# Kernel optimization log

Hardware: AMD Instinct MI355X
Metric: run time of the kernel (lower is better)

The kernel has to match this reference:

```python
import jax, jax.numpy as jnp
import numpy as np

B, S, E, H = 4, 1024, 1024, 16
D = E // H  # head_dim


def setup_inputs() -> dict:
    key = jax.random.key(0)
    ks = jax.random.split(key, 12)
    s = 1.0 / np.sqrt(E)
    return {
        "value": jax.random.normal(ks[0], (B, S, E), jnp.float32),
        "key_in": jax.random.normal(ks[1], (B, S, E), jnp.float32),
        "query": jax.random.normal(ks[2], (B, S, E), jnp.float32),
        "mask": jax.random.randint(ks[3], (B, 1, 1, S), 0, 2, jnp.int32),
        "Wq": jax.random.normal(ks[4], (E, E), jnp.float32) * s,
        "bq": jnp.zeros((E,), jnp.float32),
        "Wk": jax.random.normal(ks[5], (E, E), jnp.float32) * s,
        "bk": jnp.zeros((E,), jnp.float32),
        "Wv": jax.random.normal(ks[6], (E, E), jnp.float32) * s,
        "bv": jnp.zeros((E,), jnp.float32),
        "Wo": jax.random.normal(ks[7], (E, E), jnp.float32) * s,
        "bo": jnp.zeros((E,), jnp.float32),
    }


def reference(value, key_in, query, mask, Wq, bq, Wk, bk, Wv, bv, Wo, bo):
    b = query.shape[0]
    # torch Linear: y = x @ W.T + b
    Q = (query @ Wq.T + bq).reshape(b, query.shape[1], H, D)
    K = (key_in @ Wk.T + bk).reshape(b, key_in.shape[1], H, D)
    V = (value @ Wv.T + bv).reshape(b, value.shape[1], H, D)
    # scores scaled by 1/sqrt(embed_dim) (faithful to source, not head_dim)
    energy = jnp.einsum("bqhd,bkhd->bhqk", Q, K) / jnp.sqrt(jnp.float32(E))
    energy = jnp.where(mask == 0, jnp.float32(-1e20), energy)
    attention = jax.nn.softmax(energy, axis=-1)
    out = jnp.einsum("bhqk,bkhd->bqhd", attention, V).reshape(b, query.shape[1], E)
    return out @ Wo.T + bo
```

## Files before the change

kernel.cpp:

```cpp
#include <hip/hip_runtime.h>


typedef unsigned short u16;
typedef __bf16 bf16x8 __attribute__((ext_vector_type(8)));
typedef __bf16 bf16x2 __attribute__((ext_vector_type(2)));
typedef short s16x4 __attribute__((ext_vector_type(4)));
typedef float f32x4 __attribute__((ext_vector_type(4)));
typedef float f32x16 __attribute__((ext_vector_type(16)));

struct alignas(8) us4_t { u16 x, y, z, w; };

__device__ __forceinline__ u16 f2bf(float x) {
  unsigned int u = __builtin_bit_cast(unsigned int, x);
  unsigned int r = u + 0x7fffu + ((u >> 16) & 1u);
  return (u16)(r >> 16);
}

__device__ __forceinline__ unsigned int pack2bf(float a, float b) {
#if __has_builtin(__builtin_amdgcn_cvt_pk_bf16_f32)
  bf16x2 r = __builtin_amdgcn_cvt_pk_bf16_f32(a, b);
  return __builtin_bit_cast(unsigned int, r);
#else
  return (unsigned int)f2bf(a) | ((unsigned int)f2bf(b) << 16);
#endif
}

__device__ __forceinline__ f32x4 zero4() {
  f32x4 z; z[0] = 0.f; z[1] = 0.f; z[2] = 0.f; z[3] = 0.f; return z;
}

__device__ __forceinline__ void async_copy16(const void* g, void* l) {
  __builtin_amdgcn_global_load_lds(
      (__attribute__((address_space(1))) void*)(uintptr_t)g,
      (__attribute__((address_space(3))) void*)l, 16, 0, 0);
}

#define GATE(N)                                                         \
  do {                                                                  \
    asm volatile("s_waitcnt vmcnt(" #N ")\n\ts_barrier" ::: "memory");  \
    __builtin_amdgcn_sched_barrier(0);                                  \
  } while (0)

__global__ void fused_cast(const float* __restrict__ q, const float* __restrict__ k,
                           const float* __restrict__ v, const float* __restrict__ wq,
                           const float* __restrict__ wk, const float* __restrict__ wv,
                           const float* __restrict__ wo, const int* __restrict__ mask,
                           u16* __restrict__ qo, u16* __restrict__ ko, u16* __restrict__ vo,
                           u16* __restrict__ wqo, u16* __restrict__ wko, u16* __restrict__ wvo,
                           u16* __restrict__ woo, float* __restrict__ biasf) {
  const int blk = blockIdx.x;
  if (blk >= 16384) {
    int i = (blk - 16384) * 256 + threadIdx.x;
    biasf[i] = mask[i] ? 0.f : -1.4427e20f;
    return;
  }
  const float* src; u16* dst; int off;
  if (blk < 4096)       { src = q;  dst = qo;  off = blk; }
  else if (blk < 8192)  { src = k;  dst = ko;  off = blk - 4096; }
  else if (blk < 12288) { src = v;  dst = vo;  off = blk - 8192; }
  else if (blk < 13312) { src = wq; dst = wqo; off = blk - 12288; }
  else if (blk < 14336) { src = wk; dst = wko; off = blk - 13312; }
  else if (blk < 15360) { src = wv; dst = wvo; off = blk - 14336; }
  else                  { src = wo; dst = woo; off = blk - 15360; }
  const size_t i = (size_t)off * 256 + threadIdx.x;
  float4 f = ((const float4*)src)[i];
  unsigned int lo = pack2bf(f.x, f.y), hi = pack2bf(f.z, f.w);
  unsigned long long pk = (unsigned long long)lo | ((unsigned long long)hi << 32);
  ((unsigned long long*)dst)[i] = pk;
}

template <int MLO>
__device__ __forceinline__ void mm8(f32x16 (&acc)[4][2], const bf16x8 (&af)[2][2],
                                    const bf16x8 (&bfr)[2][2]) {
  __builtin_amdgcn_s_setprio(1);
#pragma unroll
  for (int ks = 0; ks < 2; ++ks)
#pragma unroll
    for (int mf = 0; mf < 2; ++mf)
#pragma unroll
      for (int nf = 0; nf < 2; ++nf)
        acc[MLO + mf][nf] = __builtin_amdgcn_mfma_f32_32x32x16_bf16(
            af[mf][ks], bfr[nf][ks], acc[MLO + mf][nf], 0, 0, 0);
  __builtin_amdgcn_s_setprio(0);
}

__global__ __launch_bounds__(512, 2) void qkv_gemm256(
    const u16* __restrict__ Xq, const u16* __restrict__ Xk, const u16* __restrict__ Xv,
    const u16* __restrict__ Wq, const u16* __restrict__ Wk, const u16* __restrict__ Wv,
    const float* __restrict__ bq, const float* __restrict__ bk, const float* __restrict__ bv,
    u16* __restrict__ Qo, u16* __restrict__ Ko, u16* __restrict__ Vto) {
  __shared__ u16 lA[2][2][256 * 32];
  __shared__ u16 lB[2][2][256 * 32];

  const int tid = threadIdx.x;
  const int lane = tid & 63, w = tid >> 6;
  const int wm = w >> 2, wn = w & 3;
  const int l32 = lane & 31, hi = lane >> 5;

  const int flat = blockIdx.x;
  const int xcd = flat & 7, t = flat >> 3;
  const int g = xcd * 24 + t;
  const int mt = g >> 2, n = g & 3;
  const int z = mt >> 4, m = mt & 15;
  const u16* A = (z == 0) ? Xq : (z == 1) ? Xk : Xv;
  const u16* W = (z == 0) ? Wq : (z == 1) ? Wk : Wv;
  const float* bias = (z == 0) ? bq : (z == 1) ? bk : bv;
  u16* out = (z == 0) ? Qo : (z == 1) ? Ko : Vto;
  const bool trans = (z == 2);
  const int m0 = m * 256, n0 = n * 256;

  f32x16 acc[4][2];
#pragma unroll
  for (int i = 0; i < 4; ++i)
#pragma unroll
    for (int j = 0; j < 2; ++j)
#pragma unroll
      for (int e = 0; e < 16; ++e) acc[i][j][e] = 0.f;

  int offA[2], offB[2];
#pragma unroll
  for (int t2 = 0; t2 < 2; ++t2) {
    const int row = (t2 * 8 + w) * 16 + (lane >> 2);
    const int c2 = (lane & 3) ^ ((lane >> 3) & 3);
    offA[t2] = (m0 + row) * 1024 + c2 * 8;
    offB[t2] = (n0 + row) * 1024 + c2 * 8;
  }

  const u16* cA = &lA[0][0][0];
  const u16* cB = &lB[0][0][0];
  u16* nA = (u16*)&lA[1][0][0];
  u16* nB = (u16*)&lB[1][0][0];

  auto stA = [&](u16* dst, int h, int k0) {
#pragma unroll
    for (int t2 = 0; t2 < 2; ++t2)
      async_copy16(A + (offA[t2] + k0 + h * 32), dst + h * 8192 + (t2 * 8 + w) * 512);
  };
  auto stB = [&](u16* dst, int h, int k0) {
#pragma unroll
    for (int t2 = 0; t2 < 2; ++t2)
      async_copy16(W + (offB[t2] + k0 + h * 32), dst + h * 8192 + (t2 * 8 + w) * 512);
  };
  auto rd = [&](const u16* base, int h, int row, int ks) -> bf16x8 {
    const int pc = (ks * 2 + hi) ^ ((row >> 1) & 3);
    return *(const bf16x8*)&base[h * 8192 + row * 32 + pc * 8];
  };

  stA((u16*)cA, 0, 0);
  stB((u16*)cB, 0, 0);
  stA((u16*)cA, 1, 0);
  stB((u16*)cB, 1, 0);

  bf16x8 af[2][2], bfr[2][2];
  for (int kt = 0; kt < 16; ++kt) {
    const bool st = (kt < 15);
    const int k1 = (kt + 1) * 64;

    GATE(4);
#pragma unroll
    for (int mf = 0; mf < 2; ++mf)
#pragma unroll
      for (int ks = 0; ks < 2; ++ks)
        af[mf][ks] = rd(cA, 0, wm * 128 + mf * 32 + l32, ks);
#pragma unroll
    for (int nf = 0; nf < 2; ++nf)
#pragma unroll
      for (int ks = 0; ks < 2; ++ks)
        bfr[nf][ks] = rd(cB, 0, wn * 64 + nf * 32 + l32, ks);
    if (st) stA(nA, 0, k1);
    mm8<0>(acc, af, bfr);

#pragma unroll
    for (int mf = 0; mf < 2; ++mf)
#pragma unroll
      for (int ks = 0; ks < 2; ++ks)
        af[mf][ks] = rd(cA, 0, wm * 128 + (2 + mf) * 32 + l32, ks);
    if (st) stB(nB, 0, k1);
    mm8<2>(acc, af, bfr);

    if (st) { GATE(4); } else { GATE(0); }
#pragma unroll
    for (int mf = 0; mf < 2; ++mf)
#pragma unroll
      for (int ks = 0; ks < 2; ++ks)
        af[mf][ks] = rd(cA, 1, wm * 128 + mf * 32 + l32, ks);
#pragma unroll
    for (int nf = 0; nf < 2; ++nf)
#pragma unroll
      for (int ks = 0; ks < 2; ++ks)
        bfr[nf][ks] = rd(cB, 1, wn * 64 + nf * 32 + l32, ks);
    if (st) stA(nA, 1, k1);
    mm8<0>(acc, af, bfr);

#pragma unroll
    for (int mf = 0; mf < 2; ++mf)
#pragma unroll
      for (int ks = 0; ks < 2; ++ks)
        af[mf][ks] = rd(cA, 1, wm * 128 + (2 + mf) * 32 + l32, ks);
    if (st) stB(nB, 1, k1);
    mm8<2>(acc, af, bfr);

    const u16* tA = cA; cA = nA; nA = (u16*)tA;
    const u16* tB = cB; cB = nB; nB = (u16*)tB;
  }

#pragma unroll
  for (int nf = 0; nf < 2; ++nf) {
    const int cg = n0 + wn * 64 + nf * 32 + l32;
    const float bj = bias[cg];
#pragma unroll
    for (int mf = 0; mf < 4; ++mf) {
      const int mbase = m0 + wm * 128 + mf * 32 + 4 * hi;
#pragma unroll
      for (int g2 = 0; g2 < 4; ++g2) {
        const int r0 = mbase + 8 * g2;
        if (!trans) {
#pragma unroll
          for (int rr = 0; rr < 4; ++rr)
            out[(size_t)(r0 + rr) * 1024 + cg] = f2bf(acc[mf][nf][g2 * 4 + rr] + bj);
        } else {
          const int bh = ((r0 >> 10) << 4) + (cg >> 6);
          const int gq = (r0 & 1023) >> 2;
          const int d = cg & 63;
          union { us4_t s; unsigned int u[2]; } pk;
          pk.u[0] = pack2bf(acc[mf][nf][g2 * 4 + 0] + bj, acc[mf][nf][g2 * 4 + 1] + bj);
          pk.u[1] = pack2bf(acc[mf][nf][g2 * 4 + 2] + bj, acc[mf][nf][g2 * 4 + 3] + bj);
          *(us4_t*)&out[(size_t)bh * 65536 + gq * 256 + d * 4] = pk.s;
        }
      }
    }
  }
}

template <bool OUT_BF16, int NT>
__device__ __forceinline__ void gemm_core32(const u16* __restrict__ A,
                                            const u16* __restrict__ Bw,
                                            const float* __restrict__ bias,
                                            void* __restrict__ outp, bool trans,
                                            int m0, int n0) {
  __shared__ u16 lA[128 * 64];
  __shared__ u16 lB[NT * 64 * 64];
  const int tid = threadIdx.x;
  const int lane = tid & 63, w = tid >> 6;
  const int wm = w >> 1, wn = w & 1;
  const int l32 = lane & 31, hi = lane >> 5;
  const int rg = lane >> 3, cs = lane & 7;

  f32x16 acc[2][NT];
#pragma unroll
  for (int i = 0; i < 2; ++i)
#pragma unroll
    for (int j = 0; j < NT; ++j)
#pragma unroll
      for (int e = 0; e < 16; ++e) acc[i][j][e] = 0.f;

  for (int it = 0; it < 16; ++it) {
    const int k0 = it * 64;
#pragma unroll
    for (int t = 0; t < 4; ++t) {
      const int row = w * 32 + t * 8 + rg;
      const int c = cs ^ (row & 7);
      async_copy16(A + (size_t)(m0 + row) * 1024 + k0 + c * 8, &lA[(w * 32 + t * 8) * 64]);
    }
#pragma unroll
    for (int t = 0; t < NT * 2; ++t) {
      const int row = w * (NT * 16) + t * 8 + rg;
      const int c = cs ^ (row & 7);
      async_copy16(Bw + (size_t)(n0 + row) * 1024 + k0 + c * 8,
                   &lB[(w * (NT * 16) + t * 8) * 64]);
    }
    __syncthreads();
#pragma unroll
    for (int s = 0; s < 4; ++s) {
      bf16x8 af[2], bfr[NT];
#pragma unroll
      for (int i = 0; i < 2; ++i) {
        const int row = wm * 64 + i * 32 + l32;
        af[i] = *(const bf16x8*)&lA[row * 64 + (((s * 2 + hi) ^ (row & 7)) * 8)];
      }
#pragma unroll
      for (int j = 0; j < NT; ++j) {
        const int row = wn * (NT * 32) + j * 32 + l32;
        bfr[j] = *(const bf16x8*)&lB[row * 64 + (((s * 2 + hi) ^ (row & 7)) * 8)];
      }
#pragma unroll
      for (int i = 0; i < 2; ++i)
#pragma unroll
        for (int j = 0; j < NT; ++j)
          acc[i][j] = __builtin_amdgcn_mfma_f32_32x32x16_bf16(af[i], bfr[j], acc[i][j], 0, 0, 0);
    }
    __syncthreads();
  }

#pragma unroll
  for (int j = 0; j < NT; ++j) {
    const int cg = n0 + wn * (NT * 32) + j * 32 + l32;
    const float bj = bias[cg];
#pragma unroll
    for (int i = 0; i < 2; ++i) {
      const int mbase = m0 + wm * 64 + i * 32 + 4 * hi;
#pragma unroll
      for (int g = 0; g < 4; ++g) {
        const int r0 = mbase + 8 * g;
        if (!trans) {
          if (OUT_BF16) {
            u16* o = (u16*)outp;
#pragma unroll
            for (int rr = 0; rr < 4; ++rr)
              o[(size_t)(r0 + rr) * 1024 + cg] = f2bf(acc[i][j][g * 4 + rr] + bj);
          } else {
            float* o = (float*)outp;
#pragma unroll
            for (int rr = 0; rr < 4; ++rr)
              o[(size_t)(r0 + rr) * 1024 + cg] = acc[i][j][g * 4 + rr] + bj;
          }
        } else {
          u16* o = (u16*)outp;
          const int bh = ((r0 >> 10) << 4) + (cg >> 6);
          const int g2 = (r0 & 1023) >> 2;
          const int d  = cg & 63;
          union { us4_t s; unsigned int u[2]; } pk;
          pk.u[0] = pack2bf(acc[i][j][g * 4 + 0] + bj, acc[i][j][g * 4 + 1] + bj);
          pk.u[1] = pack2bf(acc[i][j][g * 4 + 2] + bj, acc[i][j][g * 4 + 3] + bj);
          *(us4_t*)&o[(size_t)bh * 65536 + g2 * 256 + d * 4] = pk.s;
        }
      }
    }
  }
}

__global__ __launch_bounds__(256, 3) void out_gemm(
    const u16* __restrict__ A, const u16* __restrict__ W,
    const float* __restrict__ bias, float* __restrict__ out) {
  const int flat = blockIdx.x;
  const int xcd = flat & 7, t = flat >> 3;
  const int n = t & 15, m = xcd * 4 + (t >> 4);
  gemm_core32<false, 1>(A, W, bias, out, false, m * 128, n * 64);
}

__global__ __launch_bounds__(256, 4) void attn_kernel(
    const u16* __restrict__ Qb, const u16* __restrict__ Kb, const u16* __restrict__ Vtb,
    const float* __restrict__ biasf, u16* __restrict__ Ob) {
  __shared__ u16 lK[128 * 64];
  __shared__ u16 lV[64 * 128];
  u16* lQ = lV;

  const int tid = threadIdx.x;
  const int lane = tid & 63, w = tid >> 6;
  const int quad = lane >> 4, l16 = lane & 15;
  const int rg = lane >> 3, cs = lane & 7;

  const int flat = blockIdx.x;
  const int xcd = flat & 7, r = flat >> 3;
  const int bh = xcd * 8 + (r & 7), qt = r >> 3;
  const int b = bh >> 4;
  const size_t qkBase = (size_t)b * 1048576 + (size_t)(bh & 15) * 64;
  const size_t vBase = (size_t)bh * 65536;
  const float C = 0.0450842200277982f;
  const float* bp = biasf + b * 1024 + quad * 4;

#pragma unroll
  for (int t = 0; t < 2; ++t) {
    const int row = w * 16 + t * 8 + rg;
    const int c = cs ^ (row & 7);
    async_copy16(Qb + qkBase + (size_t)(qt * 64 + row) * 1024 + c * 8,
                 &lQ[(w * 16 + t * 8) * 64]);
  }
  __syncthreads();

  bf16x8 qf[2];
#pragma unroll
  for (int kk = 0; kk < 2; ++kk) {
    const int row = w * 16 + l16;
    qf[kk] = *(const bf16x8*)&lQ[row * 64 + (((kk * 4 + quad) ^ (row & 7)) * 8)];
  }
  __syncthreads();

  float lsum = 0.f;
  f32x4 oacc[4];
#pragma unroll
  for (int dt = 0; dt < 4; ++dt) oacc[dt] = zero4();

  for (int it = 0; it < 8; ++it) {
    const int k0 = it * 128;
#pragma unroll
    for (int t = 0; t < 4; ++t) {
      const int row = w * 32 + t * 8 + rg;
      const int c = cs ^ (row & 7);
      async_copy16(Kb + qkBase + (size_t)(k0 + row) * 1024 + c * 8,
                   &lK[(w * 32 + t * 8) * 64]);
    }
#pragma unroll
    for (int t = 0; t < 4; ++t) {
      const int o16 = (w * 4 + t) * 512 + lane * 8;
      async_copy16(Vtb + vBase + (size_t)it * 8192 + o16, &lV[(w * 4 + t) * 512]);
    }
    __syncthreads();

    f32x4 sacc[8];
#pragma unroll
    for (int n = 0; n < 8; ++n) sacc[n] = zero4();
#pragma unroll
    for (int kk = 0; kk < 2; ++kk) {
#pragma unroll
      for (int n = 0; n < 8; ++n) {
        const int row = n * 16 + l16;
        bf16x8 kf = *(const bf16x8*)&lK[row * 64 + (((kk * 4 + quad) ^ (row & 7)) * 8)];
        sacc[n] = __builtin_amdgcn_mfma_f32_16x16x32_bf16(kf, qf[kk], sacc[n], 0, 0, 0);
      }
    }

    f32x4 sum4 = zero4();
#pragma unroll
    for (int n = 0; n < 8; ++n) {
      const float4 vb = *(const float4*)&bp[k0 + n * 16];
      sacc[n][0] = __builtin_amdgcn_exp2f(fmaf(sacc[n][0], C, vb.x));
      sacc[n][1] = __builtin_amdgcn_exp2f(fmaf(sacc[n][1], C, vb.y));
      sacc[n][2] = __builtin_amdgcn_exp2f(fmaf(sacc[n][2], C, vb.z));
      sacc[n][3] = __builtin_amdgcn_exp2f(fmaf(sacc[n][3], C, vb.w));
      sum4[0] += sacc[n][0]; sum4[1] += sacc[n][1];
      sum4[2] += sacc[n][2]; sum4[3] += sacc[n][3];
    }
    float rs = (sum4[0] + sum4[1]) + (sum4[2] + sum4[3]);
    rs += __shfl_xor(rs, 16);
    rs += __shfl_xor(rs, 32);
    lsum += rs;

    s16x4 pf[8];
#pragma unroll
    for (int n = 0; n < 8; ++n) {
      union { s16x4 v; unsigned int u[2]; } pu;
      pu.u[0] = pack2bf(sacc[n][0], sacc[n][1]);
      pu.u[1] = pack2bf(sacc[n][2], sacc[n][3]);
      pf[n] = pu.v;
    }

#pragma unroll
    for (int dt = 0; dt < 4; ++dt) {
      const int dbase = (dt * 16 + l16) * 4;
#pragma unroll
      for (int ks = 0; ks < 8; ++ks) {
        s16x4 vf = *(const s16x4*)&lV[(ks * 4 + quad) * 256 + dbase];
        oacc[dt] = __builtin_amdgcn_mfma_f32_16x16x16bf16_1k(vf, pf[ks], oacc[dt], 0, 0, 0);
      }
    }
    __syncthreads();
  }

  const float inv = 1.f / lsum;
  const int qg = qt * 64 + w * 16 + l16;
#pragma unroll
  for (int dt = 0; dt < 4; ++dt) {
    union { us4_t s; unsigned int u[2]; } pk;
    pk.u[0] = pack2bf(oacc[dt][0] * inv, oacc[dt][1] * inv);
    pk.u[1] = pack2bf(oacc[dt][2] * inv, oacc[dt][3] * inv);
    *(us4_t*)&Ob[qkBase + (size_t)qg * 1024 + dt * 16 + quad * 4] = pk.s;
  }
}

extern "C" void kernel_launch(void* const* d_in, const int* in_sizes, int n_in,
                              void* d_out, int out_size, void* d_ws, size_t ws_size,
                              hipStream_t stream) {
  const float* value  = (const float*)d_in[0];
  const float* key_in = (const float*)d_in[1];
  const float* query  = (const float*)d_in[2];
  const int*   mask   = (const int*)d_in[3];
  const float* Wq = (const float*)d_in[4];
  const float* bq = (const float*)d_in[5];
  const float* Wk = (const float*)d_in[6];
  const float* bk = (const float*)d_in[7];
  const float* Wv = (const float*)d_in[8];
  const float* bv = (const float*)d_in[9];
  const float* Wo = (const float*)d_in[10];
  const float* bo = (const float*)d_in[11];

  u16* ws = (u16*)d_ws;
  u16* q_bf  = ws;
  u16* k_bf  = ws + 4194304;
  u16* v_bf  = ws + 8388608;
  u16* wq_bf = ws + 12582912;
  u16* wk_bf = ws + 13631488;
  u16* wv_bf = ws + 14680064;
  u16* wo_bf = ws + 15728640;
  u16* Qbuf  = ws + 16777216;
  u16* Kbuf  = ws + 20971520;
  u16* Vtbuf = ws + 25165824;
  u16* attnb = ws + 29360128;
  float* biasf = (float*)d_out;

  fused_cast<<<16400, 256, 0, stream>>>(query, key_in, value, Wq, Wk, Wv, Wo, mask,
                                        q_bf, k_bf, v_bf, wq_bf, wk_bf, wv_bf, wo_bf,
                                        biasf);
  qkv_gemm256<<<dim3(192), 512, 0, stream>>>(q_bf, k_bf, v_bf, wq_bf, wk_bf, wv_bf,
                                             bq, bk, bv, Qbuf, Kbuf, Vtbuf);
  attn_kernel<<<dim3(1024), 256, 0, stream>>>(Qbuf, Kbuf, Vtbuf, biasf, attnb);
  out_gemm<<<dim3(512), 256, 0, stream>>>(attnb, wo_bf, bo, (float*)d_out);
}
```

Measured before the change: 206.6 us.

## Register-prefetch next K/V tile during compute and raise MFMA wave priority

Replaces the per-iteration async global-to-LDS copies of K and V with loads into registers issued one iteration ahead. The registers are then written to LDS at the start of the next iteration, so global latency overlaps the score and PV MFMA work. It also wraps the MFMA sections in s_setprio to favour waves issuing matrix work. The cost is extra VGPRs for the prefetch buffers, which may reduce occupancy, plus an added LDS store pass. The odd Qb nullptr check on Kp looks like an anti-optimisation guard.

Result: slower. 271.5 us (+31.4%).

```diff
diff --git a/kernel.cpp b/kernel.cpp
--- a/kernel.cpp
+++ b/kernel.cpp
@@ -376,6 +376,23 @@
   }
   __syncthreads();
 
+  const u16* Kp = Qb == nullptr ? nullptr : Kb + qkBase;
+  const u16* Vp = Vtb + vBase;
+  int kro[4];
+#pragma unroll
+  for (int t = 0; t < 4; ++t) {
+    const int row = w * 32 + t * 8 + rg;
+    const int c = cs ^ (row & 7);
+    kro[t] = row * 1024 + c * 8;
+  }
+  const int vo = w * 2048 + lane * 8;
+
+  float4 kreg[4], vreg[4];
+#pragma unroll
+  for (int t = 0; t < 4; ++t) kreg[t] = *(const float4*)&Kp[kro[t]];
+#pragma unroll
+  for (int t = 0; t < 4; ++t) vreg[t] = *(const float4*)&Vp[vo + t * 512];
+
   float lsum = 0.f;
   f32x4 oacc[4];
 #pragma unroll
@@ -384,22 +401,26 @@
   for (int it = 0; it < 8; ++it) {
     const int k0 = it * 128;
 #pragma unroll
-    for (int t = 0; t < 4; ++t) {
-      const int row = w * 32 + t * 8 + rg;
-      const int c = cs ^ (row & 7);
-      async_copy16(Kb + qkBase + (size_t)(k0 + row) * 1024 + c * 8,
-                   &lK[(w * 32 + t * 8) * 64]);
-    }
-#pragma unroll
-    for (int t = 0; t < 4; ++t) {
-      const int o16 = (w * 4 + t) * 512 + lane * 8;
-      async_copy16(Vtb + vBase + (size_t)it * 8192 + o16, &lV[(w * 4 + t) * 512]);
-    }
+    for (int t = 0; t < 4; ++t)
+      *(float4*)&lK[(w * 32 + t * 8) * 64 + lane * 8] = kreg[t];
+#pragma unroll
+    for (int t = 0; t < 4; ++t)
+      *(float4*)&lV[(w * 4 + t) * 512 + lane * 8] = vreg[t];
     __syncthreads();
+    if (it < 7) {
+      const int kn = (it + 1) * 128;
+#pragma unroll
+      for (int t = 0; t < 4; ++t)
+        kreg[t] = *(const float4*)&Kp[(size_t)kn * 1024 + kro[t]];
+#pragma unroll
+      for (int t = 0; t < 4; ++t)
+        vreg[t] = *(const float4*)&Vp[(size_t)(it + 1) * 8192 + vo + t * 512];
+    }
 
     f32x4 sacc[8];
 #pragma unroll
     for (int n = 0; n < 8; ++n) sacc[n] = zero4();
+    __builtin_amdgcn_s_setprio(1);
 #pragma unroll
     for (int kk = 0; kk < 2; ++kk) {
 #pragma unroll
@@ -409,6 +430,7 @@
         sacc[n] = __builtin_amdgcn_mfma_f32_16x16x32_bf16(kf, qf[kk], sacc[n], 0, 0, 0);
       }
     }
+    __builtin_amdgcn_s_setprio(0);
 
     f32x4 sum4 = zero4();
 #pragma unroll
@@ -435,6 +457,7 @@
       pf[n] = pu.v;
     }
 
+    __builtin_amdgcn_s_setprio(1);
 #pragma unroll
     for (int dt = 0; dt < 4; ++dt) {
       const int dbase = (dt * 16 + l16) * 4;
@@ -444,6 +467,7 @@
         oacc[dt] = __builtin_amdgcn_mfma_f32_16x16x16bf16_1k(vf, pf[ks], oacc[dt], 0, 0, 0);
       }
     }
+    __builtin_amdgcn_s_setprio(0);
     __syncthreads();
   }
 
```

## Shrink QKV GEMM tiles to 128x128 with triple-buffered K pipeline

Applied to the files above, without the earlier changes.

The QKV projection GEMM moves from 256x256 tiles with 512 threads and double buffering to 128x128 tiles with 256 threads, a 3-stage LDS ring, and 768 blocks remapped across XCDs. The goal is better CU occupancy and load balance (192 blocks underfill the device) and deeper prefetch. Per-tile data reuse drops in exchange. Separately, the attention kernel's MFMA sections are wrapped in s_setprio raises. An unused accv array is declared.

After: 206.5 us. Within noise of the previous version (-0.0%).

```diff
diff --git a/kernel.cpp b/kernel.cpp
--- a/kernel.cpp
+++ b/kernel.cpp
@@ -69,139 +69,102 @@
   ((unsigned long long*)dst)[i] = pk;
 }
 
-template <int MLO>
-__device__ __forceinline__ void mm8(f32x16 (&acc)[4][2], const bf16x8 (&af)[2][2],
-                                    const bf16x8 (&bfr)[2][2]) {
-  __builtin_amdgcn_s_setprio(1);
-#pragma unroll
-  for (int ks = 0; ks < 2; ++ks)
-#pragma unroll
-    for (int mf = 0; mf < 2; ++mf)
-#pragma unroll
-      for (int nf = 0; nf < 2; ++nf)
-        acc[MLO + mf][nf] = __builtin_amdgcn_mfma_f32_32x32x16_bf16(
-            af[mf][ks], bfr[nf][ks], acc[MLO + mf][nf], 0, 0, 0);
-  __builtin_amdgcn_s_setprio(0);
-}
-
-__global__ __launch_bounds__(512, 2) void qkv_gemm256(
+__global__ __launch_bounds__(256, 3) void qkv_gemm128(
     const u16* __restrict__ Xq, const u16* __restrict__ Xk, const u16* __restrict__ Xv,
     const u16* __restrict__ Wq, const u16* __restrict__ Wk, const u16* __restrict__ Wv,
     const float* __restrict__ bq, const float* __restrict__ bk, const float* __restrict__ bv,
     u16* __restrict__ Qo, u16* __restrict__ Ko, u16* __restrict__ Vto) {
-  __shared__ u16 lA[2][2][256 * 32];
-  __shared__ u16 lB[2][2][256 * 32];
+  __shared__ u16 lA[3][4096];
+  __shared__ u16 lB[3][4096];
 
   const int tid = threadIdx.x;
   const int lane = tid & 63, w = tid >> 6;
-  const int wm = w >> 2, wn = w & 3;
+  const int wm = w >> 1, wn = w & 1;
   const int l32 = lane & 31, hi = lane >> 5;
 
   const int flat = blockIdx.x;
-  const int xcd = flat & 7, t = flat >> 3;
-  const int g = xcd * 24 + t;
-  const int mt = g >> 2, n = g & 3;
-  const int z = mt >> 4, m = mt & 15;
+  const int xcd = flat & 7, i = flat >> 3;
+  const int g = xcd * 96 + i;
+  const int n = g & 7, mt = g >> 3;
+  const int z = mt >> 5, m = mt & 31;
   const u16* A = (z == 0) ? Xq : (z == 1) ? Xk : Xv;
   const u16* W = (z == 0) ? Wq : (z == 1) ? Wk : Wv;
   const float* bias = (z == 0) ? bq : (z == 1) ? bk : bv;
   u16* out = (z == 0) ? Qo : (z == 1) ? Ko : Vto;
   const bool trans = (z == 2);
-  const int m0 = m * 256, n0 = n * 256;
-
-  f32x16 acc[4][2];
-#pragma unroll
-  for (int i = 0; i < 4; ++i)
-#pragma unroll
-    for (int j = 0; j < 2; ++j)
-#pragma unroll
-      for (int e = 0; e < 16; ++e) acc[i][j][e] = 0.f;
+  const int m0 = m * 128, n0 = n * 128;
+
+  f32x4 accv[2][2][4];
+  f32x16 acc[2][2];
+#pragma unroll
+  for (int a2 = 0; a2 < 2; ++a2)
+#pragma unroll
+    for (int b2 = 0; b2 < 2; ++b2)
+#pragma unroll
+      for (int e = 0; e < 16; ++e) acc[a2][b2][e] = 0.f;
+  (void)accv;
 
   int offA[2], offB[2];
 #pragma unroll
   for (int t2 = 0; t2 < 2; ++t2) {
-    const int row = (t2 * 8 + w) * 16 + (lane >> 2);
+    const int row = (t2 * 4 + w) * 16 + (lane >> 2);
     const int c2 = (lane & 3) ^ ((lane >> 3) & 3);
     offA[t2] = (m0 + row) * 1024 + c2 * 8;
     offB[t2] = (n0 + row) * 1024 + c2 * 8;
   }
 
-  const u16* cA = &lA[0][0][0];
-  const u16* cB = &lB[0][0][0];
-  u16* nA = (u16*)&lA[1][0][0];
-  u16* nB = (u16*)&lB[1][0][0];
-
-  auto stA = [&](u16* dst, int h, int k0) {
+  auto stg = [&](int buf, int s) {
+    const int k0 = s * 32;
 #pragma unroll
     for (int t2 = 0; t2 < 2; ++t2)
-      async_copy16(A + (offA[t2] + k0 + h * 32), dst + h * 8192 + (t2 * 8 + w) * 512);
+      async_copy16(A + (offA[t2] + k0), &lA[buf][(t2 * 4 + w) * 512]);
+#pragma unroll
+    for (int t2 = 0; t2 < 2; ++t2)
+      async_copy16(W + (offB[t2] + k0), &lB[buf][(t2 * 4 + w) * 512]);
   };
-  auto stB = [&](u16* dst, int h, int k0) {
-#pragma unroll
-    for (int t2 = 0; t2 < 2; ++t2)
-      async_copy16(W + (offB[t2] + k0 + h * 32), dst + h * 8192 + (t2 * 8 + w) * 512);
+  auto rdA = [&](int buf, int mf, int ks) -> bf16x8 {
+    const int row = wm * 64 + mf * 32 + l32;
+    const int pc = (ks * 2 + hi) ^ ((row >> 1) & 3);
+    return *(const bf16x8*)&lA[buf][row * 32 + pc * 8];
   };
-  auto rd = [&](const u16* base, int h, int row, int ks) -> bf16x8 {
+  auto rdB = [&](int buf, int nf, int ks) -> bf16x8 {
+    const int row = wn * 64 + nf * 32 + l32;
     const int pc = (ks * 2 + hi) ^ ((row >> 1) & 3);
-    return *(const bf16x8*)&base[h * 8192 + row * 32 + pc * 8];
+    return *(const bf16x8*)&lB[buf][row * 32 + pc * 8];
   };
 
-  stA((u16*)cA, 0, 0);
-  stB((u16*)cB, 0, 0);
-  stA((u16*)cA, 1, 0);
-  stB((u16*)cB, 1, 0);
-
-  bf16x8 af[2][2], bfr[2][2];
-  for (int kt = 0; kt < 16; ++kt) {
-    const bool st = (kt < 15);
-    const int k1 = (kt + 1) * 64;
-
-    GATE(4);
+  stg(0, 0);
+  stg(1, 1);
+
+  int cb = 0;
+  for (int s = 0; s < 32; ++s) {
+    if (s < 31) { GATE(4); } else { GATE(0); }
+    if (s < 30) {
+      int sb = cb + 2; if (sb >= 3) sb -= 3;
+      stg(sb, s + 2);
+    }
+    bf16x8 af[2][2], bfr[2][2];
 #pragma unroll
     for (int mf = 0; mf < 2; ++mf)
 #pragma unroll
       for (int ks = 0; ks < 2; ++ks)
-        af[mf][ks] = rd(cA, 0, wm * 128 + mf * 32 + l32, ks);
+        af[mf][ks] = rdA(cb, mf, ks);
 #pragma unroll
     for (int nf = 0; nf < 2; ++nf)
 #pragma unroll
       for (int ks = 0; ks < 2; ++ks)
-        bfr[nf][ks] = rd(cB, 0, wn * 64 + nf * 32 + l32, ks);
-    if (st) stA(nA, 0, k1);
-    mm8<0>(acc, af, bfr);
-
-#pragma unroll
-    for (int mf = 0; mf < 2; ++mf)
-#pragma unroll
-      for (int ks = 0; ks < 2; ++ks)
-        af[mf][ks] = rd(cA, 0, wm * 128 + (2 + mf) * 32 + l32, ks);
-    if (st) stB(nB, 0, k1);
-    mm8<2>(acc, af, bfr);
-
-    if (st) { GATE(4); } else { GATE(0); }
-#pragma unroll
-    for (int mf = 0; mf < 2; ++mf)
-#pragma unroll
-      for (int ks = 0; ks < 2; ++ks)
-        af[mf][ks] = rd(cA, 1, wm * 128 + mf * 32 + l32, ks);
-#pragma unroll
-    for (int nf = 0; nf < 2; ++nf)
-#pragma unroll
-      for (int ks = 0; ks < 2; ++ks)
-        bfr[nf][ks] = rd(cB, 1, wn * 64 + nf * 32 + l32, ks);
-    if (st) stA(nA, 1, k1);
-    mm8<0>(acc, af, bfr);
-
-#pragma unroll
-    for (int mf = 0; mf < 2; ++mf)
-#pragma unroll
-      for (int ks = 0; ks < 2; ++ks)
-        af[mf][ks] = rd(cA, 1, wm * 128 + (2 + mf) * 32 + l32, ks);
-    if (st) stB(nB, 1, k1);
-    mm8<2>(acc, af, bfr);
-
-    const u16* tA = cA; cA = nA; nA = (u16*)tA;
-    const u16* tB = cB; cB = nB; nB = (u16*)tB;
+        bfr[nf][ks] = rdB(cb, nf, ks);
+    __builtin_amdgcn_s_setprio(1);
+#pragma unroll
+    for (int ks = 0; ks < 2; ++ks)
+#pragma unroll
+      for (int mf = 0; mf < 2; ++mf)
+#pragma unroll
+        for (int nf = 0; nf < 2; ++nf)
+          acc[mf][nf] = __builtin_amdgcn_mfma_f32_32x32x16_bf16(
+              af[mf][ks], bfr[nf][ks], acc[mf][nf], 0, 0, 0);
+    __builtin_amdgcn_s_setprio(0);
+    cb = (cb == 2) ? 0 : cb + 1;
   }
 
 #pragma unroll
@@ -209,8 +172,8 @@
     const int cg = n0 + wn * 64 + nf * 32 + l32;
     const float bj = bias[cg];
 #pragma unroll
-    for (int mf = 0; mf < 4; ++mf) {
-      const int mbase = m0 + wm * 128 + mf * 32 + 4 * hi;
+    for (int mf = 0; mf < 2; ++mf) {
+      const int mbase = m0 + wm * 64 + mf * 32 + 4 * hi;
 #pragma unroll
       for (int g2 = 0; g2 < 4; ++g2) {
         const int r0 = mbase + 8 * g2;
@@ -400,6 +363,7 @@
     f32x4 sacc[8];
 #pragma unroll
     for (int n = 0; n < 8; ++n) sacc[n] = zero4();
+    __builtin_amdgcn_s_setprio(1);
 #pragma unroll
     for (int kk = 0; kk < 2; ++kk) {
 #pragma unroll
@@ -409,6 +373,7 @@
         sacc[n] = __builtin_amdgcn_mfma_f32_16x16x32_bf16(kf, qf[kk], sacc[n], 0, 0, 0);
       }
     }
+    __builtin_amdgcn_s_setprio(0);
 
     f32x4 sum4 = zero4();
 #pragma unroll
@@ -435,6 +400,7 @@
       pf[n] = pu.v;
     }
 
+    __builtin_amdgcn_s_setprio(1);
 #pragma unroll
     for (int dt = 0; dt < 4; ++dt) {
       const int dbase = (dt * 16 + l16) * 4;
@@ -444,6 +410,7 @@
         oacc[dt] = __builtin_amdgcn_mfma_f32_16x16x16bf16_1k(vf, pf[ks], oacc[dt], 0, 0, 0);
       }
     }
+    __builtin_amdgcn_s_setprio(0);
     __syncthreads();
   }
 
@@ -491,7 +458,7 @@
   fused_cast<<<16400, 256, 0, stream>>>(query, key_in, value, Wq, Wk, Wv, Wo, mask,
                                         q_bf, k_bf, v_bf, wq_bf, wk_bf, wv_bf, wo_bf,
                                         biasf);
-  qkv_gemm256<<<dim3(192), 512, 0, stream>>>(q_bf, k_bf, v_bf, wq_bf, wk_bf, wv_bf,
+  qkv_gemm128<<<dim3(768), 256, 0, stream>>>(q_bf, k_bf, v_bf, wq_bf, wk_bf, wv_bf,
                                              bq, bk, bv, Qbuf, Kbuf, Vtbuf);
   attn_kernel<<<dim3(1024), 256, 0, stream>>>(Qbuf, Kbuf, Vtbuf, biasf, attnb);
   out_gemm<<<dim3(512), 256, 0, stream>>>(attnb, wo_bf, bo, (float*)d_out);
```
